# Kernel optimization log

Hardware: AMD Instinct MI355X
Metric: run time of the kernel (lower is better)

## Reference

```python
import jax, jax.numpy as jnp
import numpy as np

N, E, D = 100000, 400000, 128

def setup_inputs() -> dict:
    key = jax.random.key(0)
    k1, k2, k3, k4, k5 = jax.random.split(key, 5)
    x = jax.random.normal(k1, (N, D), dtype=jnp.float32)
    e = jax.random.normal(k2, (E, D), dtype=jnp.float32)
    # torch nn.Linear(3D, D, bias=False) weight is [D, 3D]; we store W = weight.T -> [3D, D]
    W = jax.random.normal(k3, (3 * D, D), dtype=jnp.float32) * (1.0 / np.sqrt(3 * D))
    src_idx = jax.random.randint(k4, (E,), 0, N, dtype=jnp.int64)
    dst_idx = jax.random.randint(k5, (E,), 0, N, dtype=jnp.int64)
    return {"x": x, "e": e, "W": W, "src_idx": src_idx, "dst_idx": dst_idx}

def reference(x, e, W, src_idx, dst_idx):
    # message = Linear(concat([src_feat, tgt_feat, role_feat], -1))
    # Split W into the three d-blocks so we never materialize the [E, 3D] concat:
    # concat([a,b,c]) @ W == a@W1 + b@W2 + c@W3  (exactly the same math)
    d = x.shape[-1]
    W_src, W_dst, W_e = W[:d], W[d:2 * d], W[2 * d:]
    m = x[src_idx] @ W_src + x[dst_idx] @ W_dst + e @ W_e  # [E, D]
    return m
```

## Files before the change

### kernel.cpp

```cpp
#include <hip/hip_runtime.h>
#include <hip/hip_bf16.h>

typedef __attribute__((ext_vector_type(8))) short bf16x8;
typedef __attribute__((ext_vector_type(4))) float f32x4;

#define D128 128
#define IMG_SHORTS 16384
#define XB_OFF 65536
#define NBLK 256
#define WSH (3 * IMG_SHORTS)
#define RBS 4096

__device__ __forceinline__ short f2bf(float f) {
    union { float f; unsigned u; } v; v.f = f;
    unsigned r = (v.u + 0x7FFFu + ((v.u >> 16) & 1u)) >> 16;
    return (short)r;
}

__device__ __forceinline__ short f2bf_h(float f) {
    __hip_bfloat16 h = __float2bfloat16(f);
    short s;
    __builtin_memcpy(&s, &h, sizeof(short));
    return s;
}

__device__ __forceinline__ bf16x8 pack8(f32x4 a, f32x4 b) {
    bf16x8 r;
    r[0] = f2bf_h(a[0]); r[1] = f2bf_h(a[1]); r[2] = f2bf_h(a[2]); r[3] = f2bf_h(a[3]);
    r[4] = f2bf_h(b[0]); r[5] = f2bf_h(b[1]); r[6] = f2bf_h(b[2]); r[7] = f2bf_h(b[3]);
    return r;
}

__device__ __forceinline__ void gload_lds16(const short* g, short* l) {
    __builtin_amdgcn_global_load_lds(
        (const __attribute__((address_space(1))) unsigned int*)(const void*)g,
        (__attribute__((address_space(3))) unsigned int*)(void*)l, 16, 0, 0);
}

__global__ __launch_bounds__(256) void wt_kernel(const float* __restrict__ W,
                                                 short* __restrict__ Wimg) {
    const int c    = blockIdx.x >> 3;
    const int frag = (blockIdx.x & 7) * 4 + (threadIdx.x >> 6);
    const int lane = threadIdx.x & 63;
    const int mt = frag >> 2, ks = frag & 3;
    const int m  = mt * 16 + (lane & 15);
    const int k0 = ks * 32 + (lane >> 4) * 8;
    bf16x8 v;
#pragma unroll
    for (int j = 0; j < 8; ++j)
        v[j] = f2bf(W[(size_t)(c * 128 + k0 + j) * D128 + m]);
    *reinterpret_cast<bf16x8*>(
        &Wimg[((size_t)c * 32 + frag) * 64 * 8 + (size_t)lane * 8]) = v;
}

__global__ __launch_bounds__(256) void xb_kernel(const float* __restrict__ x,
                                                 short* __restrict__ xb) {
    const size_t i = ((size_t)blockIdx.x * 256 + threadIdx.x) * 8;
    f32x4 v0 = reinterpret_cast<const f32x4*>(x + i)[0];
    f32x4 v1 = reinterpret_cast<const f32x4*>(x + i)[1];
    *reinterpret_cast<bf16x8*>(xb + i) = pack8(v0, v1);
}

__global__ __launch_bounds__(512, 2) void fused_kernel(
        const short* __restrict__ xb,
        const float* __restrict__ e,
        const short* __restrict__ Wimg,
        const int*  __restrict__ src_idx,
        const int*  __restrict__ dst_idx,
        float* __restrict__ out,
        int E, int ntiles)
{
    __shared__ short lds[WSH + 8 * RBS];

    const int tid  = threadIdx.x;
    const int lane = tid & 63;
    const int w    = tid >> 6;
    const int r    = lane >> 2;
    const int q    = lane & 3;
    const int sx   = (r >> 1) & 3;
    const int fr   = lane & 15;
    const int lhi  = lane >> 4;
    const int rb_off = (fr * 4 + (lhi ^ ((fr >> 1) & 3))) * 8;

    short* RB = &lds[WSH + w * RBS];
    short* BB = RB + 2048;

    const int per = ntiles >> 8;
    const int rem = ntiles & 255;
    const int b   = blockIdx.x;
    const int t0  = b * per + (b < rem ? b : rem);
    const int t1  = t0 + per + (b < rem ? 1 : 0);

#pragma unroll
    for (int jj = 0; jj < 12; ++jj) {
        int unit = jj * 512 + tid;
        gload_lds16(Wimg + (size_t)unit * 8, &lds[unit * 8]);
    }
    int rp = t0 * 128 + w * 16 + r;
    int si = src_idx[rp];
    int di = dst_idx[rp];
    asm volatile("" ::: "memory");
    asm volatile("s_waitcnt vmcnt(0)" ::: "memory");
    __builtin_amdgcn_s_barrier();

    bf16x8 wa_e[24];
#pragma unroll
    for (int mt = 0; mt < 6; ++mt)
#pragma unroll
        for (int ks = 0; ks < 4; ++ks)
            wa_e[mt * 4 + ks] = *reinterpret_cast<const bf16x8*>(
                &lds[((2 * 32 + mt * 4 + ks) * 64 + lane) * 8]);

#pragma unroll
    for (int ks = 0; ks < 4; ++ks)
        gload_lds16(xb + (size_t)si * D128 + ks * 32 + (q ^ sx) * 8, &RB[ks * 512]);
    asm volatile("" ::: "memory");

    for (int t = t0; t < t1; ++t) {
        const int rn = t * 128 + w * 16 + fr;

#pragma unroll
        for (int ks = 0; ks < 4; ++ks)
            gload_lds16(xb + (size_t)di * D128 + ks * 32 + (q ^ sx) * 8,
                        &BB[ks * 512]);
        asm volatile("" ::: "memory");

        const float* pe = e + (size_t)rn * D128;
        f32x4 ev[8];
#pragma unroll
        for (int ks = 0; ks < 4; ++ks) {
            ev[2 * ks]     = reinterpret_cast<const f32x4*>(pe + ks * 32 + lhi * 8)[0];
            ev[2 * ks + 1] = reinterpret_cast<const f32x4*>(pe + ks * 32 + lhi * 8)[1];
        }
        asm volatile("" ::: "memory");

        int rpn = (t + 1) * 128 + w * 16 + r;
        if (rpn >= E) rpn = E - 1;
        const int sin_ = src_idx[rpn];
        const int din_ = dst_idx[rpn];
        asm volatile("" ::: "memory");

        asm volatile("s_waitcnt vmcnt(14)" ::: "memory");
        __builtin_amdgcn_sched_barrier(0);

        f32x4 acc[8];
#pragma unroll
        for (int mt = 0; mt < 8; ++mt) acc[mt] = (f32x4){0.f, 0.f, 0.f, 0.f};

#pragma unroll
        for (int ks = 0; ks < 4; ++ks) {
            bf16x8 bfr = *reinterpret_cast<const bf16x8*>(&RB[ks * 512 + rb_off]);
#pragma unroll
            for (int mt = 0; mt < 8; ++mt) {
                bf16x8 a = *reinterpret_cast<const bf16x8*>(
                    &lds[((0 * 32 + mt * 4 + ks) * 64 + lane) * 8]);
                acc[mt] = __builtin_amdgcn_mfma_f32_16x16x32_bf16(a, bfr, acc[mt], 0, 0, 0);
            }
        }

        asm volatile("s_waitcnt vmcnt(10)" ::: "memory");
        __builtin_amdgcn_sched_barrier(0);

#pragma unroll
        for (int ks = 0; ks < 4; ++ks) {
            bf16x8 bfr = *reinterpret_cast<const bf16x8*>(&BB[ks * 512 + rb_off]);
#pragma unroll
            for (int mt = 0; mt < 8; ++mt) {
                bf16x8 a = *reinterpret_cast<const bf16x8*>(
                    &lds[((1 * 32 + mt * 4 + ks) * 64 + lane) * 8]);
                acc[mt] = __builtin_amdgcn_mfma_f32_16x16x32_bf16(a, bfr, acc[mt], 0, 0, 0);
            }
        }
        asm volatile("" ::: "memory");

#pragma unroll
        for (int ks = 0; ks < 4; ++ks)
            gload_lds16(xb + (size_t)sin_ * D128 + ks * 32 + (q ^ sx) * 8, &RB[ks * 512]);
        asm volatile("" ::: "memory");
        si = sin_; di = din_;

        asm volatile("s_waitcnt vmcnt(6)" ::: "memory");
        __builtin_amdgcn_sched_barrier(0);

#pragma unroll
        for (int ks = 0; ks < 4; ++ks) {
            bf16x8 be = pack8(ev[2 * ks], ev[2 * ks + 1]);
#pragma unroll
            for (int mt = 0; mt < 6; ++mt)
                acc[mt] = __builtin_amdgcn_mfma_f32_16x16x32_bf16(
                    wa_e[mt * 4 + ks], be, acc[mt], 0, 0, 0);
#pragma unroll
            for (int mt = 6; mt < 8; ++mt) {
                bf16x8 a = *reinterpret_cast<const bf16x8*>(
                    &lds[((2 * 32 + mt * 4 + ks) * 64 + lane) * 8]);
                acc[mt] = __builtin_amdgcn_mfma_f32_16x16x32_bf16(a, be, acc[mt], 0, 0, 0);
            }
        }

        float* po = out + (size_t)rn * D128 + lhi * 4;
#pragma unroll
        for (int mt = 0; mt < 8; ++mt)
            *reinterpret_cast<f32x4*>(po + mt * 16) = acc[mt];
        asm volatile("" ::: "memory");
    }
}

extern "C" void kernel_launch(void* const* d_in, const int* in_sizes, int n_in,
                              void* d_out, int out_size, void* d_ws, size_t ws_size,
                              hipStream_t stream) {
    const float* x = (const float*)d_in[0];
    const float* e = (const float*)d_in[1];
    const float* W = (const float*)d_in[2];
    const int* src = (const int*)d_in[3];
    const int* dst = (const int*)d_in[4];
    float* out = (float*)d_out;

    short* Wimg = (short*)d_ws;
    short* xb   = (short*)d_ws + XB_OFF;

    const int N = in_sizes[0] / D128;
    const int E = in_sizes[3];
    const int ntiles = E / 128;

    wt_kernel<<<24, 256, 0, stream>>>(W, Wimg);
    xb_kernel<<<(N * D128) / (256 * 8), 256, 0, stream>>>(x, xb);
    fused_kernel<<<NBLK, 512, 0, stream>>>(xb, e, Wimg, src, dst, out, E, ntiles);
}
```

Before: 128.8 us.

## Replace async global-to-LDS gathers with register-staged loads and deeper prefetch

Gathered x rows for src and dst now go through registers, with explicit LDS stores, instead of async global_load_lds. The e rows and the next indices are prefetched one tile ahead at the end of each iteration. Hand-placed vmcnt waits are removed in favour of compiler-managed dependencies. The 24 register-cached W_e fragments are dropped and read from LDS, freeing registers for the staged loads but adding LDS reads.

Measured after the change: 133.8 us. 1.04x slower.

```diff
diff --git a/kernel.cpp b/kernel.cpp
--- a/kernel.cpp
+++ b/kernel.cpp
@@ -96,24 +96,31 @@
         int unit = jj * 512 + tid;
         gload_lds16(Wimg + (size_t)unit * 8, &lds[unit * 8]);
     }
+    asm volatile("" ::: "memory");
+    asm volatile("s_waitcnt vmcnt(0)" ::: "memory");
+    __builtin_amdgcn_s_barrier();
+
     int rp = t0 * 128 + w * 16 + r;
     int si = src_idx[rp];
     int di = dst_idx[rp];
-    asm volatile("" ::: "memory");
-    asm volatile("s_waitcnt vmcnt(0)" ::: "memory");
-    __builtin_amdgcn_s_barrier();
-
-    bf16x8 wa_e[24];
-#pragma unroll
-    for (int mt = 0; mt < 6; ++mt)
-#pragma unroll
-        for (int ks = 0; ks < 4; ++ks)
-            wa_e[mt * 4 + ks] = *reinterpret_cast<const bf16x8*>(
-                &lds[((2 * 32 + mt * 4 + ks) * 64 + lane) * 8]);
-
+    bf16x8 sl[4];
 #pragma unroll
     for (int ks = 0; ks < 4; ++ks)
-        gload_lds16(xb + (size_t)si * D128 + ks * 32 + (q ^ sx) * 8, &RB[ks * 512]);
+        sl[ks] = *reinterpret_cast<const bf16x8*>(
+            xb + (size_t)si * D128 + ks * 32 + (q ^ sx) * 8);
+    f32x4 ev[8];
+    {
+        const float* pe = e + (size_t)(t0 * 128 + w * 16 + fr) * D128;
+#pragma unroll
+        for (int ks = 0; ks < 4; ++ks) {
+            ev[2 * ks]     = reinterpret_cast<const f32x4*>(pe + ks * 32 + lhi * 8)[0];
+            ev[2 * ks + 1] = reinterpret_cast<const f32x4*>(pe + ks * 32 + lhi * 8)[1];
+        }
+    }
+    int rpn = (t0 + 1) * 128 + w * 16 + r;
+    if (rpn >= E) rpn = E - 1;
+    int sn = src_idx[rpn];
+    int dn = dst_idx[rpn];
     asm volatile("" ::: "memory");
 
     for (int t = t0; t < t1; ++t) {
@@ -121,27 +128,19 @@
 
 #pragma unroll
         for (int ks = 0; ks < 4; ++ks)
-            gload_lds16(xb + (size_t)di * D128 + ks * 32 + (q ^ sx) * 8,
-                        &BB[ks * 512]);
-        asm volatile("" ::: "memory");
-
-        const float* pe = e + (size_t)rn * D128;
-        f32x4 ev[8];
-#pragma unroll
-        for (int ks = 0; ks < 4; ++ks) {
-            ev[2 * ks]     = reinterpret_cast<const f32x4*>(pe + ks * 32 + lhi * 8)[0];
-            ev[2 * ks + 1] = reinterpret_cast<const f32x4*>(pe + ks * 32 + lhi * 8)[1];
-        }
-        asm volatile("" ::: "memory");
-
-        int rpn = (t + 1) * 128 + w * 16 + r;
-        if (rpn >= E) rpn = E - 1;
-        const int sin_ = src_idx[rpn];
-        const int din_ = dst_idx[rpn];
-        asm volatile("" ::: "memory");
-
-        asm volatile("s_waitcnt vmcnt(14)" ::: "memory");
-        __builtin_amdgcn_sched_barrier(0);
+            *reinterpret_cast<bf16x8*>(&RB[ks * 512 + lane * 8]) = sl[ks];
+        asm volatile("" ::: "memory");
+
+        bf16x8 dl[4];
+#pragma unroll
+        for (int ks = 0; ks < 4; ++ks)
+            dl[ks] = *reinterpret_cast<const bf16x8*>(
+                xb + (size_t)di * D128 + ks * 32 + (q ^ sx) * 8);
+#pragma unroll
+        for (int ks = 0; ks < 4; ++ks)
+            sl[ks] = *reinterpret_cast<const bf16x8*>(
+                xb + (size_t)sn * D128 + ks * 32 + (q ^ sx) * 8);
+        asm volatile("" ::: "memory");
 
         f32x4 acc[8];
 #pragma unroll
@@ -157,9 +156,12 @@
                 acc[mt] = __builtin_amdgcn_mfma_f32_16x16x32_bf16(a, bfr, acc[mt], 0, 0, 0);
             }
         }
-
-        asm volatile("s_waitcnt vmcnt(10)" ::: "memory");
-        __builtin_amdgcn_sched_barrier(0);
+        asm volatile("" ::: "memory");
+
+#pragma unroll
+        for (int ks = 0; ks < 4; ++ks)
+            *reinterpret_cast<bf16x8*>(&BB[ks * 512 + lane * 8]) = dl[ks];
+        asm volatile("" ::: "memory");
 
 #pragma unroll
         for (int ks = 0; ks < 4; ++ks) {
@@ -171,26 +173,12 @@
                 acc[mt] = __builtin_amdgcn_mfma_f32_16x16x32_bf16(a, bfr, acc[mt], 0, 0, 0);
             }
         }
-        asm volatile("" ::: "memory");
-
-#pragma unroll
-        for (int ks = 0; ks < 4; ++ks)
-            gload_lds16(xb + (size_t)sin_ * D128 + ks * 32 + (q ^ sx) * 8, &RB[ks * 512]);
-        asm volatile("" ::: "memory");
-        si = sin_; di = din_;
-
-        asm volatile("s_waitcnt vmcnt(6)" ::: "memory");
-        __builtin_amdgcn_sched_barrier(0);
 
 #pragma unroll
         for (int ks = 0; ks < 4; ++ks) {
             bf16x8 be = pack8(ev[2 * ks], ev[2 * ks + 1]);
 #pragma unroll
-            for (int mt = 0; mt < 6; ++mt)
-                acc[mt] = __builtin_amdgcn_mfma_f32_16x16x32_bf16(
-                    wa_e[mt * 4 + ks], be, acc[mt], 0, 0, 0);
-#pragma unroll
-            for (int mt = 6; mt < 8; ++mt) {
+            for (int mt = 0; mt < 8; ++mt) {
                 bf16x8 a = *reinterpret_cast<const bf16x8*>(
                     &lds[((2 * 32 + mt * 4 + ks) * 64 + lane) * 8]);
                 acc[mt] = __builtin_amdgcn_mfma_f32_16x16x32_bf16(a, be, acc[mt], 0, 0, 0);
@@ -201,6 +189,23 @@
 #pragma unroll
         for (int mt = 0; mt < 8; ++mt)
             *reinterpret_cast<f32x4*>(po + mt * 16) = acc[mt];
+        asm volatile("" ::: "memory");
+
+        di = dn;
+        {
+            int ern = (t + 1) * 128 + w * 16 + fr;
+            if (ern >= E) ern = E - 1;
+            const float* pe = e + (size_t)ern * D128;
+#pragma unroll
+            for (int ks = 0; ks < 4; ++ks) {
+                ev[2 * ks]     = reinterpret_cast<const f32x4*>(pe + ks * 32 + lhi * 8)[0];
+                ev[2 * ks + 1] = reinterpret_cast<const f32x4*>(pe + ks * 32 + lhi * 8)[1];
+            }
+        }
+        int rp2 = (t + 2) * 128 + w * 16 + r;
+        if (rp2 >= E) rp2 = E - 1;
+        sn = src_idx[rp2];
+        dn = dst_idx[rp2];
         asm volatile("" ::: "memory");
     }
 }
```
